# Kernel optimization log

Hardware: AMD Instinct MI355X
Metric: run time of the kernel (lower is better)

Reference implementation:

```python
import jax, jax.numpy as jnp
import numpy as np

N, E, D, G, FP = 20000, 320000, 1280, 64, 65


def _glorot(k, shape):
    s = jnp.sqrt(6.0 / (shape[0] + shape[1])).astype(jnp.float32)
    return jax.random.uniform(k, shape, jnp.float32, -s, s)


def setup_inputs() -> dict:
    key = jax.random.key(0)
    ks = jax.random.split(key, 16)
    return {
        'x': jax.random.normal(ks[0], (N, D), jnp.float32),
        'edge_index': jax.random.randint(ks[1], (2, E), 0, N),
        'batch': jnp.sort(jax.random.randint(ks[2], (N,), 0, G)),
        'fp_x': jax.random.normal(ks[3], (G, FP), jnp.float32),
        'W1': _glorot(ks[4], (D, D)), 'b1': jnp.zeros((D,), jnp.float32),
        'W2': _glorot(ks[5], (D, 640)), 'b2': jnp.zeros((640,), jnp.float32),
        'W3': _glorot(ks[6], (640, 320)), 'b3': jnp.zeros((320,), jnp.float32),
        'Wg1': _glorot(ks[7], (320, 1024)), 'bg1': jnp.zeros((1024,), jnp.float32),
        'Wg2': _glorot(ks[8], (1024, 128)), 'bg2': jnp.zeros((128,), jnp.float32),
        'Wf1': _glorot(ks[9], (193, 1024)), 'bf1': jnp.zeros((1024,), jnp.float32),
        'Wf2': _glorot(ks[10], (1024, 512)), 'bf2': jnp.zeros((512,), jnp.float32),
        'Wo': _glorot(ks[11], (512, 1)), 'bo': jnp.zeros((1,), jnp.float32),
    }


def reference(x, edge_index, batch, fp_x, W1, b1, W2, b2, W3, b3,
              Wg1, bg1, Wg2, bg2, Wf1, bf1, Wf2, bf2, Wo, bo):
    n = x.shape[0]
    g = fp_x.shape[0]
    loop = jnp.arange(n)
    src = jnp.concatenate([edge_index[0], loop])  # self-loops added (GCNConv default)
    dst = jnp.concatenate([edge_index[1], loop])
    deg = jax.ops.segment_sum(jnp.ones_like(dst, x.dtype), dst, num_segments=n)
    dis = jnp.where(deg > 0, jax.lax.rsqrt(deg), 0.0)
    norm = dis[src] * dis[dst]  # D^-1/2 (A+I) D^-1/2 edge weights

    def gcn(h, W, b):
        h = h @ W                                  # transform first (PyG GCNConv)
        agg = jax.ops.segment_sum(h[src] * norm[:, None], dst, num_segments=n)
        return agg + b

    xt = jax.nn.relu(gcn(x, W1, b1))
    xt = jax.nn.relu(gcn(xt, W2, b2))
    xt = jax.nn.relu(gcn(xt, W3, b3))
    # global mean pool over graphs
    s = jax.ops.segment_sum(xt, batch, num_segments=g)
    cnt = jax.ops.segment_sum(jnp.ones((n,), xt.dtype), batch, num_segments=g)
    xt = s / jnp.maximum(cnt, 1.0)[:, None]
    # MLP head (dropout in eval mode -> identity)
    xt = jax.nn.relu(xt @ Wg1 + bg1)
    xt = xt @ Wg2 + bg2
    xc = jnp.concatenate([fp_x, xt], axis=1)       # [G, 65+128=193]
    xc = jax.nn.relu(xc @ Wf1 + bf1)
    xc = jax.nn.relu(xc @ Wf2 + bf2)
    return xc @ Wo + bo
```

## Files before the change

### kernel.cpp

```cpp
#include <hip/hip_runtime.h>
#include <hip/hip_bf16.h>

#define N_NODES 20000
#define NPAD    20224
#define N_EDGES 320000
#define NGRAPH  64
#define FPD     65

typedef __attribute__((ext_vector_type(8))) __bf16 bf16x8;
typedef __attribute__((ext_vector_type(4))) float floatx4;
typedef __attribute__((ext_vector_type(8))) ushort ushort8v;

__device__ inline float bf2f(ushort u) {
    union { unsigned int i; float f; } c; c.i = ((unsigned int)u) << 16; return c.f;
}
__device__ inline ushort f2bf(float v) {
    __hip_bfloat16 h = __float2bfloat16(v);
    return *(ushort*)&h;
}
__device__ __forceinline__ void gld_lds16(const ushort* g, ushort* l) {
    __builtin_amdgcn_global_load_lds(
        (const __attribute__((address_space(1))) unsigned int*)g,
        (__attribute__((address_space(3))) unsigned int*)l,
        16, 0, 0);
}

__global__ void init_cnt(int* cnt) {
    int i = blockIdx.x * blockDim.x + threadIdx.x;
    if (i < N_NODES) cnt[i] = 1;
}
__global__ void count_in(const int* __restrict__ dst, int* cnt) {
    int e = blockIdx.x * blockDim.x + threadIdx.x;
    if (e < N_EDGES) atomicAdd(&cnt[dst[e]], 1);
}
__global__ void make_dis(const int* __restrict__ cnt, float* dis) {
    int i = blockIdx.x * blockDim.x + threadIdx.x;
    if (i < N_NODES) dis[i] = rsqrtf((float)cnt[i]);
}
__global__ __launch_bounds__(256) void scan_offsets(const int* __restrict__ cnt,
                                                    int* __restrict__ off, int* __restrict__ cursor) {
    __shared__ int part[256];
    int t = threadIdx.x;
    const int chunk = (N_NODES + 255) / 256;
    int lo = t * chunk, hi = min(lo + chunk, N_NODES);
    int s = 0;
    for (int i = lo; i < hi; ++i) s += (cnt[i] + 3) & ~3;
    part[t] = s;
    __syncthreads();
    for (int d = 1; d < 256; d <<= 1) {
        int v = (t >= d) ? part[t - d] : 0;
        __syncthreads();
        part[t] += v;
        __syncthreads();
    }
    int base = part[t] - s;
    for (int i = lo; i < hi; ++i) {
        off[i] = base; cursor[i] = base;
        base += (cnt[i] + 3) & ~3;
    }
    if (t == 255) off[N_NODES] = part[255];
}
__global__ void fill_csr(const int* __restrict__ src, const int* __restrict__ dst,
                         const float* __restrict__ dis, int* cursor,
                         int* __restrict__ esrc, float* __restrict__ ew) {
    int e = blockIdx.x * blockDim.x + threadIdx.x;
    if (e >= N_EDGES + N_NODES) return;
    int s, d; float w;
    if (e < N_EDGES) { s = src[e]; d = dst[e]; w = dis[s] * dis[d]; }
    else { s = d = e - N_EDGES; w = dis[s] * dis[s]; }
    int pos = atomicAdd(&cursor[d], 1);
    esrc[pos] = s; ew[pos] = w;
}
__global__ void fill_pad(const int* __restrict__ off, const int* __restrict__ cursor,
                         int* __restrict__ esrc, float* __restrict__ ew) {
    int i = blockIdx.x * blockDim.x + threadIdx.x;
    if (i >= N_NODES) return;
    int e1 = off[i + 1];
    for (int e = cursor[i]; e < e1; ++e) { esrc[e] = i; ew[e] = 0.f; }
}

__global__ void conv_f32_bf16_tiled(const float* __restrict__ in, ushort* __restrict__ out) {
    int idx = blockIdx.x * blockDim.x + threadIdx.x;
    if (idx >= N_NODES * 320) return;
    int n = idx / 320, f4 = idx % 320;
    float4 v = *(const float4*)(in + (size_t)n * 1280 + f4 * 4);
    ushort4 o;
    o.x = f2bf(v.x); o.y = f2bf(v.y); o.z = f2bf(v.z); o.w = f2bf(v.w);
    *(ushort4*)(out + (size_t)(f4 >> 4) * (NPAD * 64) + (size_t)n * 64 + (f4 & 15) * 4) = o;
}
__global__ void transpose_conv(const float* __restrict__ W, ushort* __restrict__ Wt,
                               int K, int Nc, int KP) {
    __shared__ float t[32][33];
    int k0 = blockIdx.x * 32, n0 = blockIdx.y * 32;
    int tx = threadIdx.x, ty = threadIdx.y;
    #pragma unroll
    for (int i = 0; i < 4; ++i)
        t[ty + i * 8][tx] = W[(size_t)(k0 + ty + i * 8) * Nc + n0 + tx];
    __syncthreads();
    #pragma unroll
    for (int i = 0; i < 4; ++i)
        Wt[(size_t)(n0 + ty + i * 8) * KP + k0 + tx] = f2bf(t[tx][ty + i * 8]);
}

__device__ __forceinline__ int swz(int r) { return (r + (r >> 2)) & 3; }

__global__ __launch_bounds__(256) void gemm_bf16_128(
    const ushort* __restrict__ A, const ushort* __restrict__ Bt,
    ushort* __restrict__ C, int M, int K, int KP, int Nc, int nt, int total, int chunk)
{
    __shared__ ushort As[128 * 32];
    __shared__ ushort Bs[128 * 32];
    const int bi = blockIdx.x;
    const int tile = (bi & 7) * chunk + (bi >> 3);
    if (tile >= total) return;
    const int bm = (tile / nt) * 128, bn = (tile % nt) * 128;

    const int tid = threadIdx.x;
    const int wid = tid >> 6, lane = tid & 63;
    const int wr = wid >> 1, wc = wid & 1;
    const int quad = lane >> 4, mr = lane & 15;

    floatx4 acc[4][4];
    #pragma unroll
    for (int i = 0; i < 4; ++i)
        #pragma unroll
        for (int j = 0; j < 4; ++j)
            acc[i][j] = (floatx4){0.f, 0.f, 0.f, 0.f};

    for (int k0 = 0; k0 < K; k0 += 32) {
        const ushort* Ak = A + (size_t)(k0 >> 6) * (NPAD * 64) + (k0 & 63);
        #pragma unroll
        for (int i = 0; i < 2; ++i) {
            int c = tid + i * 256;
            int row = c >> 2;
            int q = (c & 3) ^ swz(row);
            gld_lds16(Ak + (size_t)(bm + row) * 64 + q * 8, &As[c * 8]);
        }
        #pragma unroll
        for (int i = 0; i < 2; ++i) {
            int c = tid + i * 256;
            int row = c >> 2;
            int q = (c & 3) ^ swz(row);
            gld_lds16(Bt + (size_t)(bn + row) * KP + k0 + q * 8, &Bs[c * 8]);
        }
        __syncthreads();

        bf16x8 af[4], bfv[4];
        #pragma unroll
        for (int t = 0; t < 4; ++t) {
            int ra = wr * 64 + t * 16 + mr;
            af[t] = *(const bf16x8*)&As[ra * 32 + (quad ^ swz(ra)) * 8];
            int rb = wc * 64 + t * 16 + mr;
            bfv[t] = *(const bf16x8*)&Bs[rb * 32 + (quad ^ swz(rb)) * 8];
        }

        #pragma unroll
        for (int tm = 0; tm < 4; ++tm)
            #pragma unroll
            for (int tn = 0; tn < 4; ++tn)
                acc[tm][tn] = __builtin_amdgcn_mfma_f32_16x16x32_bf16(af[tm], bfv[tn], acc[tm][tn], 0, 0, 0);
        __syncthreads();
    }

    ushort* Cc = C + (size_t)((bn >> 6) + wc) * (NPAD * 64);
    #pragma unroll
    for (int tm = 0; tm < 4; ++tm) {
        int rowb = bm + wr * 64 + tm * 16 + quad * 4;
        #pragma unroll
        for (int r = 0; r < 4; ++r) {
            int row = rowb + r;
            if (row < M) {
                #pragma unroll
                for (int tn = 0; tn < 4; ++tn)
                    Cc[(size_t)row * 64 + tn * 16 + mr] = f2bf(acc[tm][tn][r]);
            }
        }
    }
}

__global__ __launch_bounds__(256) void gemm_bf16(
    const ushort* __restrict__ A, const ushort* __restrict__ Bt,
    ushort* __restrict__ C, int M, int K, int KP, int Nc, int nt, int total, int chunk)
{
    __shared__ ushort As[256 * 32];
    __shared__ ushort Bs[64 * 32];
    const int bi = blockIdx.x;
    const int tile = (bi & 7) * chunk + (bi >> 3);
    if (tile >= total) return;
    const int bm = (tile / nt) * 256, bn = (tile % nt) * 64;

    const int tid = threadIdx.x;
    const int wid = tid >> 6, lane = tid & 63;
    const int quad = lane >> 4, mr = lane & 15;

    floatx4 acc[4][4];
    #pragma unroll
    for (int i = 0; i < 4; ++i)
        #pragma unroll
        for (int j = 0; j < 4; ++j)
            acc[i][j] = (floatx4){0.f, 0.f, 0.f, 0.f};

    for (int k0 = 0; k0 < K; k0 += 32) {
        const ushort* Ak = A + (size_t)(k0 >> 6) * (NPAD * 64) + (k0 & 63);
        #pragma unroll
        for (int i = 0; i < 4; ++i) {
            int c = tid + i * 256;
            int row = c >> 2;
            int q = (c & 3) ^ swz(row);
            gld_lds16(Ak + (size_t)(bm + row) * 64 + q * 8, &As[c * 8]);
        }
        {
            int row = tid >> 2;
            int q = (tid & 3) ^ swz(row);
            gld_lds16(Bt + (size_t)(bn + row) * KP + k0 + q * 8, &Bs[tid * 8]);
        }
        __syncthreads();

        bf16x8 af[4], bfv[4];
        #pragma unroll
        for (int t = 0; t < 4; ++t) {
            int ra = wid * 64 + t * 16 + mr;
            af[t] = *(const bf16x8*)&As[ra * 32 + (quad ^ swz(ra)) * 8];
        }
        #pragma unroll
        for (int t = 0; t < 4; ++t) {
            int rb = t * 16 + mr;
            bfv[t] = *(const bf16x8*)&Bs[rb * 32 + (quad ^ swz(rb)) * 8];
        }

        #pragma unroll
        for (int tm = 0; tm < 4; ++tm)
            #pragma unroll
            for (int tn = 0; tn < 4; ++tn)
                acc[tm][tn] = __builtin_amdgcn_mfma_f32_16x16x32_bf16(af[tm], bfv[tn], acc[tm][tn], 0, 0, 0);
        __syncthreads();
    }

    ushort* Cc = C + (size_t)(bn >> 6) * (NPAD * 64);
    #pragma unroll
    for (int tm = 0; tm < 4; ++tm) {
        int rowb = bm + wid * 64 + tm * 16 + quad * 4;
        #pragma unroll
        for (int r = 0; r < 4; ++r) {
            int row = rowb + r;
            if (row < M) {
                #pragma unroll
                for (int tn = 0; tn < 4; ++tn)
                    Cc[(size_t)row * 64 + tn * 16 + mr] = f2bf(acc[tm][tn][r]);
            }
        }
    }
}

static inline void launch_gemm(const ushort* A, const ushort* Bt, ushort* C,
                               int M, int K, int KP, int Nc, hipStream_t stream) {
    if (Nc % 128 == 0) {
        int mt = (M + 127) / 128, nt = Nc / 128;
        int total = mt * nt;
        int chunk = (total + 7) / 8;
        gemm_bf16_128<<<8 * chunk, 256, 0, stream>>>(A, Bt, C, M, K, KP, Nc, nt, total, chunk);
    } else {
        int mt = (M + 255) / 256, nt = Nc / 64;
        int total = mt * nt;
        int chunk = (total + 7) / 8;
        gemm_bf16<<<8 * chunk, 256, 0, stream>>>(A, Bt, C, M, K, KP, Nc, nt, total, chunk);
    }
}

template<int TPN>
__global__ __launch_bounds__(256) void gather_tiled(
    const ushort* __restrict__ h, const int* __restrict__ off,
    const int* __restrict__ esrc, const float* __restrict__ ew,
    const float* __restrict__ bias, ushort* __restrict__ out_bf,
    float* __restrict__ out_f32, int wbf, int wf32, int nchunks, int nbpc)
{
    constexpr int NPB = 256 / TPN;
    const int bi = blockIdx.x;
    const int xcd = bi & 7;
    const int t2 = bi >> 3;
    const int s = t2 / nbpc, nb = t2 - s * nbpc;
    const int c = s * 8 + xcd;
    if (c >= nchunks) return;
    const int tid = threadIdx.x;
    const int g = tid / TPN, t = tid % TPN;
    const int n = nb * NPB + g;
    if (n >= N_NODES) return;

    const ushort* hc = h + (size_t)c * (NPAD * 64) + t * 8;
    float acc[8];
    #pragma unroll
    for (int j = 0; j < 8; ++j) acc[j] = 0.f;

    const int e0 = off[n], e1 = off[n + 1];
    for (int e = e0; e < e1; e += 4) {
        int4   s4 = *(const int4*)(esrc + e);
        float4 w4 = *(const float4*)(ew + e);
        ushort8v v0 = *(const ushort8v*)(hc + (size_t)s4.x * 64);
        ushort8v v1 = *(const ushort8v*)(hc + (size_t)s4.y * 64);
        ushort8v v2 = *(const ushort8v*)(hc + (size_t)s4.z * 64);
        ushort8v v3 = *(const ushort8v*)(hc + (size_t)s4.w * 64);
        #pragma unroll
        for (int j = 0; j < 8; ++j)
            acc[j] += w4.x * bf2f(v0[j]) + w4.y * bf2f(v1[j])
                    + w4.z * bf2f(v2[j]) + w4.w * bf2f(v3[j]);
    }

    const int fb = c * 64 + t * 8;
    float4 b0 = *(const float4*)(bias + fb);
    float4 b1 = *(const float4*)(bias + fb + 4);
    float r[8];
    r[0] = fmaxf(acc[0] + b0.x, 0.f); r[1] = fmaxf(acc[1] + b0.y, 0.f);
    r[2] = fmaxf(acc[2] + b0.z, 0.f); r[3] = fmaxf(acc[3] + b0.w, 0.f);
    r[4] = fmaxf(acc[4] + b1.x, 0.f); r[5] = fmaxf(acc[5] + b1.y, 0.f);
    r[6] = fmaxf(acc[6] + b1.z, 0.f); r[7] = fmaxf(acc[7] + b1.w, 0.f);
    if (wbf) {
        ushort8v o;
        #pragma unroll
        for (int j = 0; j < 8; ++j) o[j] = f2bf(r[j]);
        *(ushort8v*)(out_bf + (size_t)c * (NPAD * 64) + (size_t)n * 64 + t * 8) = o;
    }
    if (wf32) {
        *(float4*)(out_f32 + (size_t)n * (nchunks * 64) + fb)     = make_float4(r[0], r[1], r[2], r[3]);
        *(float4*)(out_f32 + (size_t)n * (nchunks * 64) + fb + 4) = make_float4(r[4], r[5], r[6], r[7]);
    }
}

static inline void launch_gather(const ushort* h, const int* off, const int* esrc,
                                 const float* ew, const float* bias, ushort* out_bf,
                                 float* out_f32, int wbf, int wf32, int nchunks,
                                 hipStream_t stream) {
    constexpr int TPN = 8;
    constexpr int NPB = 256 / TPN;
    const int nbpc = (N_NODES + NPB - 1) / NPB;
    const int sblocks = (nchunks + 7) / 8;
    gather_tiled<TPN><<<8 * sblocks * nbpc, 256, 0, stream>>>(
        h, off, esrc, ew, bias, out_bf, out_f32, wbf, wf32, nchunks, nbpc);
}

__global__ void graph_bounds(const int* __restrict__ batch, int* __restrict__ gstart) {
    int n = blockIdx.x * blockDim.x + threadIdx.x;
    if (n >= N_NODES) return;
    int b = batch[n];
    int bp = (n == 0) ? -1 : batch[n - 1];
    for (int g = bp + 1; g <= b; ++g) gstart[g] = n;
    if (n == N_NODES - 1)
        for (int g = b + 1; g <= NGRAPH; ++g) gstart[g] = N_NODES;
}
__global__ __launch_bounds__(320) void pool_graph(
    const float* __restrict__ x, const int* __restrict__ gstart, float* __restrict__ pool)
{
    int g = blockIdx.x;
    int t = threadIdx.x;
    int s = gstart[g], e = gstart[g + 1];
    float a0 = 0.f, a1 = 0.f, a2 = 0.f, a3 = 0.f;
    int n = s;
    for (; n + 3 < e; n += 4) {
        a0 += x[(size_t)(n + 0) * 320 + t];
        a1 += x[(size_t)(n + 1) * 320 + t];
        a2 += x[(size_t)(n + 2) * 320 + t];
        a3 += x[(size_t)(n + 3) * 320 + t];
    }
    for (; n < e; ++n) a0 += x[(size_t)n * 320 + t];
    float acc = (a0 + a1) + (a2 + a3);
    pool[g * 320 + t] = acc / fmaxf((float)(e - s), 1.0f);
}

template<int K, int SPLIT, int RELU>
__global__ __launch_bounds__(256) void head_gemm_sk(
    const float* __restrict__ in, int istride,
    const float* __restrict__ W, const float* __restrict__ b,
    float* __restrict__ out, int M, int Nc)
{
    constexpr int KQ = K / SPLIT;
    int idx = blockIdx.x * blockDim.x + threadIdx.x;
    int oi = idx / SPLIT, r = idx % SPLIT;
    if (oi >= M * Nc) return;
    int m = oi / Nc, c = oi % Nc;
    const float* ip = in + (size_t)m * istride + r * KQ;
    const float* wp = W + (size_t)r * KQ * Nc + c;
    float a0 = 0.f, a1 = 0.f, a2 = 0.f, a3 = 0.f;
    #pragma unroll
    for (int k = 0; k < KQ; k += 4) {
        float4 v = *(const float4*)(ip + k);
        a0 += v.x * wp[(size_t)(k + 0) * Nc];
        a1 += v.y * wp[(size_t)(k + 1) * Nc];
        a2 += v.z * wp[(size_t)(k + 2) * Nc];
        a3 += v.w * wp[(size_t)(k + 3) * Nc];
    }
    float s = (a0 + a1) + (a2 + a3);
    #pragma unroll
    for (int o = 1; o < SPLIT; o <<= 1) s += __shfl_xor(s, o, 64);
    if (r == 0) {
        s += b[c];
        out[oi] = RELU ? fmaxf(s, 0.f) : s;
    }
}

__global__ void concat_pad(const float* __restrict__ fp, const float* __restrict__ xt,
                           float* __restrict__ xc) {
    int idx = blockIdx.x * blockDim.x + threadIdx.x;
    if (idx >= NGRAPH * 208) return;
    int g = idx / 208, j = idx % 208;
    float v = 0.f;
    if (j < FPD) v = fp[g * FPD + j];
    else if (j < 193) v = xt[g * 128 + (j - FPD)];
    xc[idx] = v;
}
__global__ void pad_w(const float* __restrict__ Wf1, float* __restrict__ Wp) {
    int idx = blockIdx.x * blockDim.x + threadIdx.x;
    if (idx >= 208 * 1024) return;
    int k = idx / 1024;
    Wp[idx] = (k < 193) ? Wf1[idx] : 0.f;
}

__global__ __launch_bounds__(256) void head_out(
    const float* __restrict__ f2, const float* __restrict__ Wo,
    const float* __restrict__ bo, float* __restrict__ out)
{
    int m = blockIdx.x;
    int t = threadIdx.x;
    float2 v = *(const float2*)(f2 + (size_t)m * 512 + t * 2);
    float2 w = *(const float2*)(Wo + t * 2);
    float s = v.x * w.x + v.y * w.y;
    #pragma unroll
    for (int o = 32; o > 0; o >>= 1) s += __shfl_down(s, o, 64);
    __shared__ float ps[4];
    if ((t & 63) == 0) ps[t >> 6] = s;
    __syncthreads();
    if (t == 0) out[m] = ps[0] + ps[1] + ps[2] + ps[3] + bo[0];
}

extern "C" void kernel_launch(void* const* d_in, const int* in_sizes, int n_in,
                              void* d_out, int out_size, void* d_ws, size_t ws_size,
                              hipStream_t stream) {
    const float* x    = (const float*)d_in[0];
    const int*   eidx = (const int*)d_in[1];
    const int*   batch= (const int*)d_in[2];
    const float* fp_x = (const float*)d_in[3];
    const float* W1 = (const float*)d_in[4];  const float* b1 = (const float*)d_in[5];
    const float* W2 = (const float*)d_in[6];  const float* b2 = (const float*)d_in[7];
    const float* W3 = (const float*)d_in[8];  const float* b3 = (const float*)d_in[9];
    const float* Wg1= (const float*)d_in[10]; const float* bg1= (const float*)d_in[11];
    const float* Wg2= (const float*)d_in[12]; const float* bg2= (const float*)d_in[13];
    const float* Wf1= (const float*)d_in[14]; const float* bf1= (const float*)d_in[15];
    const float* Wf2= (const float*)d_in[16]; const float* bf2= (const float*)d_in[17];
    const float* Wo = (const float*)d_in[18]; const float* bo = (const float*)d_in[19];
    float* out = (float*)d_out;

    const int* src = eidx;
    const int* dst = eidx + N_EDGES;

    char* p = (char*)d_ws;
    float* dis   = (float*)p;  p += 20480 * 4;
    int*   cntI  = (int*)p;    p += 20480 * 4;
    int*   off   = (int*)p;    p += 20480 * 4;
    int*   cursor= (int*)p;    p += 20480 * 4;
    int*   gstart= (int*)p;    p += 128 * 4;
    int*   esrc  = (int*)p;    p += 402432 * 4;
    float* ew    = (float*)p;  p += 402432 * 4;
    ushort* xbf  = (ushort*)p; p += (size_t)NPAD * 1280 * 2;
    ushort* hbf  = (ushort*)p; p += (size_t)NPAD * 1280 * 2;
    ushort* abf  = (ushort*)p; p += (size_t)NPAD * 1280 * 2;
    float* a3f   = (float*)p;  p += (size_t)N_NODES * 320 * 4;
    ushort* Wt   = (ushort*)p; p += (size_t)1280 * 1344 * 2;
    float* pool  = (float*)p;  p += NGRAPH * 320 * 4;
    float* m1    = (float*)p;  p += NGRAPH * 1024 * 4;
    float* m2    = (float*)p;  p += NGRAPH * 128 * 4;
    float* xc    = (float*)p;  p += NGRAPH * 208 * 4;
    float* f1    = (float*)p;  p += NGRAPH * 1024 * 4;
    float* f2    = (float*)p;  p += NGRAPH * 512 * 4;
    float* Wf1p  = (float*)p;  p += 208 * 1024 * 4;

    init_cnt<<<(N_NODES + 255) / 256, 256, 0, stream>>>(cntI);
    count_in<<<(N_EDGES + 255) / 256, 256, 0, stream>>>(dst, cntI);
    make_dis<<<(N_NODES + 255) / 256, 256, 0, stream>>>(cntI, dis);
    scan_offsets<<<1, 256, 0, stream>>>(cntI, off, cursor);
    fill_csr<<<(N_EDGES + N_NODES + 255) / 256, 256, 0, stream>>>(src, dst, dis, cursor, esrc, ew);
    fill_pad<<<(N_NODES + 255) / 256, 256, 0, stream>>>(off, cursor, esrc, ew);
    graph_bounds<<<(N_NODES + 255) / 256, 256, 0, stream>>>(batch, gstart);

    {
        conv_f32_bf16_tiled<<<(N_NODES * 320 + 255) / 256, 256, 0, stream>>>(x, xbf);
        transpose_conv<<<dim3(1280 / 32, 1280 / 32), dim3(32, 8), 0, stream>>>(W1, Wt, 1280, 1280, 1344);
        launch_gemm(xbf, Wt, hbf, N_NODES, 1280, 1344, 1280, stream);
        launch_gather(hbf, off, esrc, ew, b1, abf, (float*)nullptr, 1, 0, 20, stream);
    }
    {
        transpose_conv<<<dim3(1280 / 32, 640 / 32), dim3(32, 8), 0, stream>>>(W2, Wt, 1280, 640, 1344);
        launch_gemm(abf, Wt, hbf, N_NODES, 1280, 1344, 640, stream);
        launch_gather(hbf, off, esrc, ew, b2, abf, (float*)nullptr, 1, 0, 10, stream);
    }
    {
        transpose_conv<<<dim3(640 / 32, 320 / 32), dim3(32, 8), 0, stream>>>(W3, Wt, 640, 320, 704);
        launch_gemm(abf, Wt, hbf, N_NODES, 640, 704, 320, stream);
        launch_gather(hbf, off, esrc, ew, b3, (ushort*)nullptr, a3f, 0, 1, 5, stream);
    }

    pool_graph<<<NGRAPH, 320, 0, stream>>>(a3f, gstart, pool);

    head_gemm_sk<320, 4, 1><<<(NGRAPH * 1024 * 4 + 255) / 256, 256, 0, stream>>>(pool, 320, Wg1, bg1, m1, NGRAPH, 1024);
    head_gemm_sk<1024, 8, 0><<<(NGRAPH * 128 * 8 + 255) / 256, 256, 0, stream>>>(m1, 1024, Wg2, bg2, m2, NGRAPH, 128);
    concat_pad<<<(NGRAPH * 208 + 255) / 256, 256, 0, stream>>>(fp_x, m2, xc);
    pad_w<<<(208 * 1024 + 255) / 256, 256, 0, stream>>>(Wf1, Wf1p);
    head_gemm_sk<208, 4, 1><<<(NGRAPH * 1024 * 4 + 255) / 256, 256, 0, stream>>>(xc, 208, Wf1p, bf1, f1, NGRAPH, 1024);
    head_gemm_sk<1024, 8, 1><<<(NGRAPH * 512 * 8 + 255) / 256, 256, 0, stream>>>(f1, 1024, Wf2, bf2, f2, NGRAPH, 512);
    head_out<<<NGRAPH, 256, 0, stream>>>(f2, Wo, bo, out);
}
```

Before: 757.7 us.

## Double GEMM K-step to 64 with XOR swizzle and fuse small prep kernels

Both bf16 GEMM kernels now stage 64-wide K slices per iteration instead of 32, which halves the number of barrier pairs and loop iterations. They use a row-xor-8 LDS swizzle, with two MFMA sub-steps per stage. The rsqrt degree computation is folded into the single-block scan kernel, and the concat and weight-pad kernels are merged into one launch. The GEMMs use twice the LDS per block, which may reduce occupancy, and the degree rsqrt now runs in a single block.

```diff
diff --git a/kernel.cpp b/kernel.cpp
--- a/kernel.cpp
+++ b/kernel.cpp
@@ -33,12 +33,9 @@
     int e = blockIdx.x * blockDim.x + threadIdx.x;
     if (e < N_EDGES) atomicAdd(&cnt[dst[e]], 1);
 }
-__global__ void make_dis(const int* __restrict__ cnt, float* dis) {
-    int i = blockIdx.x * blockDim.x + threadIdx.x;
-    if (i < N_NODES) dis[i] = rsqrtf((float)cnt[i]);
-}
 __global__ __launch_bounds__(256) void scan_offsets(const int* __restrict__ cnt,
-                                                    int* __restrict__ off, int* __restrict__ cursor) {
+                                                    int* __restrict__ off, int* __restrict__ cursor,
+                                                    float* __restrict__ dis) {
     __shared__ int part[256];
     int t = threadIdx.x;
     const int chunk = (N_NODES + 255) / 256;
@@ -55,8 +52,10 @@
     }
     int base = part[t] - s;
     for (int i = lo; i < hi; ++i) {
+        int c = cnt[i];
         off[i] = base; cursor[i] = base;
-        base += (cnt[i] + 3) & ~3;
+        dis[i] = rsqrtf((float)c);
+        base += (c + 3) & ~3;
     }
     if (t == 255) off[N_NODES] = part[255];
 }
@@ -102,14 +101,12 @@
         Wt[(size_t)(n0 + ty + i * 8) * KP + k0 + tx] = f2bf(t[tx][ty + i * 8]);
 }
 
-__device__ __forceinline__ int swz(int r) { return (r + (r >> 2)) & 3; }
-
 __global__ __launch_bounds__(256) void gemm_bf16_128(
     const ushort* __restrict__ A, const ushort* __restrict__ Bt,
     ushort* __restrict__ C, int M, int K, int KP, int Nc, int nt, int total, int chunk)
 {
-    __shared__ ushort As[128 * 32];
-    __shared__ ushort Bs[128 * 32];
+    __shared__ ushort As[128 * 64];
+    __shared__ ushort Bs[128 * 64];
     const int bi = blockIdx.x;
     const int tile = (bi & 7) * chunk + (bi >> 3);
     if (tile >= total) return;
@@ -127,38 +124,38 @@
         for (int j = 0; j < 4; ++j)
             acc[i][j] = (floatx4){0.f, 0.f, 0.f, 0.f};
 
-    for (int k0 = 0; k0 < K; k0 += 32) {
-        const ushort* Ak = A + (size_t)(k0 >> 6) * (NPAD * 64) + (k0 & 63);
-        #pragma unroll
-        for (int i = 0; i < 2; ++i) {
+    for (int k0 = 0; k0 < K; k0 += 64) {
+        const ushort* Ak = A + (size_t)(k0 >> 6) * (NPAD * 64);
+        #pragma unroll
+        for (int i = 0; i < 4; ++i) {
             int c = tid + i * 256;
-            int row = c >> 2;
-            int q = (c & 3) ^ swz(row);
-            gld_lds16(Ak + (size_t)(bm + row) * 64 + q * 8, &As[c * 8]);
-        }
-        #pragma unroll
-        for (int i = 0; i < 2; ++i) {
+            int row = c >> 3, g = c & 7;
+            gld_lds16(Ak + (size_t)(bm + row) * 64 + (g ^ (row & 7)) * 8, &As[c * 8]);
+        }
+        #pragma unroll
+        for (int i = 0; i < 4; ++i) {
             int c = tid + i * 256;
-            int row = c >> 2;
-            int q = (c & 3) ^ swz(row);
-            gld_lds16(Bt + (size_t)(bn + row) * KP + k0 + q * 8, &Bs[c * 8]);
+            int row = c >> 3, g = c & 7;
+            gld_lds16(Bt + (size_t)(bn + row) * KP + k0 + (g ^ (row & 7)) * 8, &Bs[c * 8]);
         }
         __syncthreads();
 
-        bf16x8 af[4], bfv[4];
-        #pragma unroll
-        for (int t = 0; t < 4; ++t) {
-            int ra = wr * 64 + t * 16 + mr;
-            af[t] = *(const bf16x8*)&As[ra * 32 + (quad ^ swz(ra)) * 8];
-            int rb = wc * 64 + t * 16 + mr;
-            bfv[t] = *(const bf16x8*)&Bs[rb * 32 + (quad ^ swz(rb)) * 8];
-        }
-
-        #pragma unroll
-        for (int tm = 0; tm < 4; ++tm)
+        #pragma unroll
+        for (int ks = 0; ks < 2; ++ks) {
+            bf16x8 af[4], bfv[4];
             #pragma unroll
-            for (int tn = 0; tn < 4; ++tn)
-                acc[tm][tn] = __builtin_amdgcn_mfma_f32_16x16x32_bf16(af[tm], bfv[tn], acc[tm][tn], 0, 0, 0);
+            for (int t = 0; t < 4; ++t) {
+                int ra = wr * 64 + t * 16 + mr;
+                af[t] = *(const bf16x8*)&As[ra * 64 + ((ks * 4 + quad) ^ (ra & 7)) * 8];
+                int rb = wc * 64 + t * 16 + mr;
+                bfv[t] = *(const bf16x8*)&Bs[rb * 64 + ((ks * 4 + quad) ^ (rb & 7)) * 8];
+            }
+            #pragma unroll
+            for (int tm = 0; tm < 4; ++tm)
+                #pragma unroll
+                for (int tn = 0; tn < 4; ++tn)
+                    acc[tm][tn] = __builtin_amdgcn_mfma_f32_16x16x32_bf16(af[tm], bfv[tn], acc[tm][tn], 0, 0, 0);
+        }
         __syncthreads();
     }
 
@@ -182,8 +179,8 @@
     const ushort* __restrict__ A, const ushort* __restrict__ Bt,
     ushort* __restrict__ C, int M, int K, int KP, int Nc, int nt, int total, int chunk)
 {
-    __shared__ ushort As[256 * 32];
-    __shared__ ushort Bs[64 * 32];
+    __shared__ ushort As[256 * 64];
+    __shared__ ushort Bs[64 * 64];
     const int bi = blockIdx.x;
     const int tile = (bi & 7) * chunk + (bi >> 3);
     if (tile >= total) return;
@@ -200,39 +197,38 @@
         for (int j = 0; j < 4; ++j)
             acc[i][j] = (floatx4){0.f, 0.f, 0.f, 0.f};
 
-    for (int k0 = 0; k0 < K; k0 += 32) {
-        const ushort* Ak = A + (size_t)(k0 >> 6) * (NPAD * 64) + (k0 & 63);
-        #pragma unroll
-        for (int i = 0; i < 4; ++i) {
+    for (int k0 = 0; k0 < K; k0 += 64) {
+        const ushort* Ak = A + (size_t)(k0 >> 6) * (NPAD * 64);
+        #pragma unroll
+        for (int i = 0; i < 8; ++i) {
             int c = tid + i * 256;
-            int row = c >> 2;
-            int q = (c & 3) ^ swz(row);
-            gld_lds16(Ak + (size_t)(bm + row) * 64 + q * 8, &As[c * 8]);
-        }
-        {
-            int row = tid >> 2;
-            int q = (tid & 3) ^ swz(row);
-            gld_lds16(Bt + (size_t)(bn + row) * KP + k0 + q * 8, &Bs[tid * 8]);
+            int row = c >> 3, g = c & 7;
+            gld_lds16(Ak + (size_t)(bm + row) * 64 + (g ^ (row & 7)) * 8, &As[c * 8]);
+        }
+        #pragma unroll
+        for (int i = 0; i < 2; ++i) {
+            int c = tid + i * 256;
+            int row = c >> 3, g = c & 7;
+            gld_lds16(Bt + (size_t)(bn + row) * KP + k0 + (g ^ (row & 7)) * 8, &Bs[c * 8]);
         }
         __syncthreads();
 
-        bf16x8 af[4], bfv[4];
-        #pragma unroll
-        for (int t = 0; t < 4; ++t) {
-            int ra = wid * 64 + t * 16 + mr;
-            af[t] = *(const bf16x8*)&As[ra * 32 + (quad ^ swz(ra)) * 8];
-        }
-        #pragma unroll
-        for (int t = 0; t < 4; ++t) {
-            int rb = t * 16 + mr;
-            bfv[t] = *(const bf16x8*)&Bs[rb * 32 + (quad ^ swz(rb)) * 8];
-        }
-
-        #pragma unroll
-        for (int tm = 0; tm < 4; ++tm)
+        #pragma unroll
+        for (int ks = 0; ks < 2; ++ks) {
+            bf16x8 af[4], bfv[4];
             #pragma unroll
-            for (int tn = 0; tn < 4; ++tn)
-                acc[tm][tn] = __builtin_amdgcn_mfma_f32_16x16x32_bf16(af[tm], bfv[tn], acc[tm][tn], 0, 0, 0);
+            for (int t = 0; t < 4; ++t) {
+                int ra = wid * 64 + t * 16 + mr;
+                af[t] = *(const bf16x8*)&As[ra * 64 + ((ks * 4 + quad) ^ (ra & 7)) * 8];
+                int rb = t * 16 + mr;
+                bfv[t] = *(const bf16x8*)&Bs[rb * 64 + ((ks * 4 + quad) ^ (rb & 7)) * 8];
+            }
+            #pragma unroll
+            for (int tm = 0; tm < 4; ++tm)
+                #pragma unroll
+                for (int tn = 0; tn < 4; ++tn)
+                    acc[tm][tn] = __builtin_amdgcn_mfma_f32_16x16x32_bf16(af[tm], bfv[tn], acc[tm][tn], 0, 0, 0);
+        }
         __syncthreads();
     }
 
@@ -396,21 +392,21 @@
     }
 }
 
-__global__ void concat_pad(const float* __restrict__ fp, const float* __restrict__ xt,
-                           float* __restrict__ xc) {
+__global__ void head_prep(const float* __restrict__ fp, const float* __restrict__ xt,
+                          float* __restrict__ xc, const float* __restrict__ Wf1,
+                          float* __restrict__ Wp) {
     int idx = blockIdx.x * blockDim.x + threadIdx.x;
-    if (idx >= NGRAPH * 208) return;
-    int g = idx / 208, j = idx % 208;
-    float v = 0.f;
-    if (j < FPD) v = fp[g * FPD + j];
-    else if (j < 193) v = xt[g * 128 + (j - FPD)];
-    xc[idx] = v;
-}
-__global__ void pad_w(const float* __restrict__ Wf1, float* __restrict__ Wp) {
-    int idx = blockIdx.x * blockDim.x + threadIdx.x;
-    if (idx >= 208 * 1024) return;
-    int k = idx / 1024;
-    Wp[idx] = (k < 193) ? Wf1[idx] : 0.f;
+    if (idx < 208 * 1024) {
+        int k = idx / 1024;
+        Wp[idx] = (k < 193) ? Wf1[idx] : 0.f;
+    }
+    if (idx < NGRAPH * 208) {
+        int g = idx / 208, j = idx % 208;
+        float v = 0.f;
+        if (j < FPD) v = fp[g * FPD + j];
+        else if (j < 193) v = xt[g * 128 + (j - FPD)];
+        xc[idx] = v;
+    }
 }
 
 __global__ __launch_bounds__(256) void head_out(
@@ -473,8 +469,7 @@
 
     init_cnt<<<(N_NODES + 255) / 256, 256, 0, stream>>>(cntI);
     count_in<<<(N_EDGES + 255) / 256, 256, 0, stream>>>(dst, cntI);
-    make_dis<<<(N_NODES + 255) / 256, 256, 0, stream>>>(cntI, dis);
-    scan_offsets<<<1, 256, 0, stream>>>(cntI, off, cursor);
+    scan_offsets<<<1, 256, 0, stream>>>(cntI, off, cursor, dis);
     fill_csr<<<(N_EDGES + N_NODES + 255) / 256, 256, 0, stream>>>(src, dst, dis, cursor, esrc, ew);
     fill_pad<<<(N_NODES + 255) / 256, 256, 0, stream>>>(off, cursor, esrc, ew);
     graph_bounds<<<(N_NODES + 255) / 256, 256, 0, stream>>>(batch, gstart);
@@ -500,8 +495,7 @@
 
     head_gemm_sk<320, 4, 1><<<(NGRAPH * 1024 * 4 + 255) / 256, 256, 0, stream>>>(pool, 320, Wg1, bg1, m1, NGRAPH, 1024);
     head_gemm_sk<1024, 8, 0><<<(NGRAPH * 128 * 8 + 255) / 256, 256, 0, stream>>>(m1, 1024, Wg2, bg2, m2, NGRAPH, 128);
-    concat_pad<<<(NGRAPH * 208 + 255) / 256, 256, 0, stream>>>(fp_x, m2, xc);
-    pad_w<<<(208 * 1024 + 255) / 256, 256, 0, stream>>>(Wf1, Wf1p);
+    head_prep<<<(208 * 1024 + 255) / 256, 256, 0, stream>>>(fp_x, m2, xc, Wf1, Wf1p);
     head_gemm_sk<208, 4, 1><<<(NGRAPH * 1024 * 4 + 255) / 256, 256, 0, stream>>>(xc, 208, Wf1p, bf1, f1, NGRAPH, 1024);
     head_gemm_sk<1024, 8, 1><<<(NGRAPH * 512 * 8 + 255) / 256, 256, 0, stream>>>(f1, 1024, Wf2, bf2, f2, NGRAPH, 512);
     head_out<<<NGRAPH, 256, 0, stream>>>(f2, Wo, bo, out);
```

Result: faster. 724.5 us (-4.4%).
